# Performance work log

Measured on AMD Instinct MI355X. Metric: run time of the kernel, lower is better.

The kernel has to match this reference:

```python
import jax, jax.numpy as jnp
import numpy as np

V, E, H, T, C, B, S = 50000, 256, 512, 50, 5, 128, 512
FC1 = 500


def setup_inputs() -> dict:
    key = jax.random.key(0)
    ks = jax.random.split(key, 13)
    n = lambda i, shape, sc: (jax.random.normal(ks[i], shape, jnp.float32) * sc)
    return {
        "x": jax.random.randint(ks[0], (B, S), 0, V),
        "topic": n(1, (B, T), 1.0),
        "h0": n(2, (B, H), 1.0),
        "c0": n(3, (B, H), 1.0),
        "embed": n(4, (V, E), 0.05),
        "W_x": n(5, (E, 4 * H), 0.02),
        "W_t": n(6, (T, 4 * H), 0.02),
        "W_h": n(7, (H, 4 * H), 0.02),
        "b": jnp.zeros((4 * H,), jnp.float32),
        "fc1_w": n(8, (FC1, H), 0.02),
        "fc1_b": jnp.zeros((FC1,), jnp.float32),
        "fc2_w": n(9, (C, FC1), 0.02),
        "fc2_b": jnp.zeros((C,), jnp.float32),
    }


def reference(x, topic, h0, c0, embed, W_x, W_t, W_h, b, fc1_w, fc1_b, fc2_w, fc2_b):
    # Embedding lookup: [B,S,E] -> time-major [S,B,E]
    x_emb = jnp.transpose(embed[x], (1, 0, 2))
    # Precompute input + topic gate contributions (topic is constant per step)
    gx = jnp.einsum("sbe,eg->sbg", x_emb, W_x) + (topic @ W_t + b)[None]  # [S,B,4H]

    def step(carry, g):
        h, c = carry
        g = g + h @ W_h
        i, f, gg, o = jnp.split(g, 4, axis=-1)
        i = jax.nn.sigmoid(i)
        f = jax.nn.sigmoid(f)
        gg = jnp.tanh(gg)
        o = jax.nn.sigmoid(o)
        c = f * c + i * gg
        h = o * jnp.tanh(c)
        return (h, c), None

    (h_last, _), _ = jax.lax.scan(step, (h0, c0), gx)
    # MLP head (dropout = identity in eval)
    hid = h_last @ fc1_w.T + fc1_b
    logits = hid @ fc2_w.T + fc2_b
    return logits
```

## Files before the change

### kernel.cpp

```cpp
#include <hip/hip_runtime.h>
#include <hip/hip_bf16.h>

typedef unsigned short u16;
typedef unsigned int u32;
typedef __attribute__((ext_vector_type(8))) short short8;
typedef __attribute__((ext_vector_type(4))) float f32x4;


__device__ __forceinline__ float bf2f(u16 v){ union{u32 u; float f;} x; x.u = ((u32)v)<<16; return x.f; }
__device__ __forceinline__ u16 f2bf(float f){ union{float f; u32 u;} x; x.f = f; u32 r = ((x.u>>16)&1u) + 0x7FFFu; return (u16)((x.u + r)>>16); }
__device__ __forceinline__ float sigf(float x){ return 1.f/(1.f+__expf(-x)); }
__device__ __forceinline__ float tanh_f(float x){ return 2.f/(1.f+__expf(-2.f*x)) - 1.f; }

#define POLL_GUARD (1u<<14)


__global__ void k_prep(const float* __restrict__ Wh, const float* __restrict__ Wx,
                       u16* __restrict__ WhT, u16* __restrict__ WxT){
  __shared__ u16 tile[32][33];
  int b = blockIdx.x;
  const float* src; u16* dst; int K, kt, nt;
  if (b < 1024){ src = Wh; dst = WhT; K = 512; kt = b & 15; nt = b >> 4; }
  else { b -= 1024; src = Wx; dst = WxT; K = 256; kt = b & 7; nt = b >> 3; }
  int tx = threadIdx.x, ty = threadIdx.y;
  #pragma unroll
  for (int p = 0; p < 4; ++p){
    int r = p*8 + ty;
    tile[r][tx] = f2bf(src[(kt*32 + r)*2048 + nt*32 + tx]);
  }
  __syncthreads();
  #pragma unroll
  for (int p = 0; p < 4; ++p){
    int r = p*8 + ty;
    dst[(nt*32 + r)*K + kt*32 + tx] = tile[tx][r];
  }
}

__global__ void k_topic(const float* __restrict__ topic, const float* __restrict__ Wt,
                        const float* __restrict__ bias, float* __restrict__ tb){
  int b = blockIdx.y;
  int col = blockIdx.x*256 + threadIdx.x;
  float acc = bias[col];
  #pragma unroll 5
  for (int t = 0; t < 50; ++t)
    acc += topic[b*50 + t] * Wt[t*2048 + col];
  tb[b*2048 + col] = acc;
}

__global__ void k_init(const float* __restrict__ h0, u32* __restrict__ U){
  int uid = blockIdx.x*256 + threadIdx.x;
  int parity = (uid >= 12288) ? 1 : 0;
  int rem = uid - parity*12288;
  int g   = rem / 768;   int r2 = rem - g*768;
  int row = r2 / 96;     int p3 = r2 - row*96;
  int prod = p3 / 6;     int u  = p3 - prod*6;
  u32 d0=0, d1=0, d2=0, d3;
  if (parity == 0){
    const float* hr = h0 + (g*8 + row)*512 + prod*32 + u*6;
    int nv = 32 - u*6; if (nv > 6) nv = 6;
    u16 vals[6] = {0,0,0,0,0,0};
    for (int j = 0; j < nv; ++j) vals[j] = f2bf(hr[j]);
    d0 = (u32)vals[0] | ((u32)vals[1]<<16);
    d1 = (u32)vals[2] | ((u32)vals[3]<<16);
    d2 = (u32)vals[4] | ((u32)vals[5]<<16);
    d3 = 0u;
  } else {
    d3 = 0xFFFFFFFFu;
  }
  u32* dst = U + (size_t)uid*4;
  dst[0]=d0; dst[1]=d1; dst[2]=d2; dst[3]=d3;
}

__global__ void __launch_bounds__(256, 1)
k_rnn(const int* __restrict__ x, const float* __restrict__ embed, const float* __restrict__ c0,
      const u16* __restrict__ WhT, const u16* __restrict__ WxT, const float* __restrict__ tb,
      u32* __restrict__ U, float* __restrict__ hf)
{
  const int bx = blockIdx.x;
  const int g = bx & 15;
  const int w = bx >> 4;
  const int tid = threadIdx.x;
  const int v = tid >> 6;
  const int lane = tid & 63;
  const int l15 = lane & 15, l4 = lane >> 4;
  const int arr = l15 & 7;

  __shared__ __align__(16) u16 ldsH[8][704];
  __shared__ __align__(16) float ldsD[16][132];
  __shared__ int ldsX[8][512];
  __shared__ u16 ldsP[8][32];

  const int er = tid >> 5, ehc = tid & 31;
  const int eb = g*8 + er;
  const int ecol = w*32 + ehc;
  float c_val = c0[eb*512 + ecol];
  const float tb0 = tb[eb*2048 +    0 + ecol];
  const float tb1 = tb[eb*2048 +  512 + ecol];
  const float tb2 = tb[eb*2048 + 1024 + ecol];
  const float tb3 = tb[eb*2048 + 1536 + ecol];

  short8 b2[2][16], b1[2][8];
  #pragma unroll
  for (int j = 0; j < 2; ++j){
    const int cl = (2*v + j)*16 + l15;
    const int cg = (cl & 3)*512 + w*32 + (cl >> 2);
    #pragma unroll
    for (int kt = 0; kt < 16; ++kt)
      b2[j][kt] = *(const short8*)(WhT + cg*512 + kt*32 + l4*8);
    #pragma unroll
    for (int kt = 0; kt < 8; ++kt)
      b1[j][kt] = *(const short8*)(WxT + cg*256 + kt*32 + l4*8);
  }

  {
    const int4* src = (const int4*)(x + g*4096);
    int4* dst = (int4*)&ldsX[0][0];
    #pragma unroll
    for (int i = 0; i < 4; ++i) dst[tid + 256*i] = src[tid + 256*i];
  }
  __syncthreads();

  int rw0,rw1,rw2, cb0,cb1,cb2; u32 of0,of1,of2;
  {
    int pid, row, p3, prod, u;
    pid = tid*3 + 0; row = pid/96; p3 = pid - row*96; prod = p3/6; u = p3 - prod*6;
    rw0 = row; cb0 = prod*40 + u*6 + row*8; of0 = (u32)(((g*8+row)*16+prod)*6+u);
    pid = tid*3 + 1; row = pid/96; p3 = pid - row*96; prod = p3/6; u = p3 - prod*6;
    rw1 = row; cb1 = prod*40 + u*6 + row*8; of1 = (u32)(((g*8+row)*16+prod)*6+u);
    pid = tid*3 + 2; row = pid/96; p3 = pid - row*96; prod = p3/6; u = p3 - prod*6;
    rw2 = row; cb2 = prod*40 + u*6 + row*8; of2 = (u32)(((g*8+row)*16+prod)*6+u);
  }
  int pk_row=0, pk_ucol=0, pk_nv=0; u32 pk_off=0;
  if (tid < 48){
    pk_row = tid/6; int u = tid - pk_row*6;
    pk_ucol = u*6;
    pk_nv = 32 - pk_ucol; if (pk_nv > 6) pk_nv = 6;
    pk_off = (u32)(((g*8+pk_row)*16 + w)*6 + u);
  }
  int goff[16];
  #pragma unroll
  for (int kt = 0; kt < 16; ++kt) goff[kt] = kt*40 + l4*8 + arr*8;
  const u16* hrow = &ldsH[arr][0];

  short8 a1A[8], a1B[8];
  {
    const int idx0 = ldsX[arr][0];
    const float* ep = embed + (u32)idx0*256 + l4*8;
    #pragma unroll
    for (int kt = 0; kt < 8; ++kt){
      float4 f0 = *(const float4*)(ep + kt*32);
      float4 f1 = *(const float4*)(ep + kt*32 + 4);
      union { short8 s; u32 u[4]; } pk;
      asm("v_cvt_pk_bf16_f32 %0, %1, %2" : "=v"(pk.u[0]) : "v"(f0.x), "v"(f0.y));
      asm("v_cvt_pk_bf16_f32 %0, %1, %2" : "=v"(pk.u[1]) : "v"(f0.z), "v"(f0.w));
      asm("v_cvt_pk_bf16_f32 %0, %1, %2" : "=v"(pk.u[2]) : "v"(f1.x), "v"(f1.y));
      asm("v_cvt_pk_bf16_f32 %0, %1, %2" : "=v"(pk.u[3]) : "v"(f1.z), "v"(f1.w));
      a1A[kt] = pk.s;
    }
  }

  union F4 { f32x4 f; u32 u[4]; };

  auto step = [&](int t, short8 (&a1c)[8], short8 (&a1n)[8]){
    const int tn = (t < 511) ? t + 1 : 511;
    const int idxn = ldsX[arr][tn];
    const float* ep = embed + (u32)idxn*256 + l4*8;
    f32x4 e[16];
    #pragma unroll
    for (int kt = 0; kt < 8; ++kt){
      asm volatile("global_load_dwordx4 %0, %2, off\n\t"
                   "global_load_dwordx4 %1, %3, off"
                   : "=v"(e[2*kt]), "=v"(e[2*kt+1])
                   : "v"(ep + kt*32), "v"(ep + kt*32 + 4));
    }
    f32x4 aX0a = {0.f,0.f,0.f,0.f}, aX0b = {0.f,0.f,0.f,0.f};
    f32x4 aX1a = {0.f,0.f,0.f,0.f}, aX1b = {0.f,0.f,0.f,0.f};
    #pragma unroll
    for (int kt = 0; kt < 4; ++kt){
      aX0a = __builtin_amdgcn_mfma_f32_16x16x32_bf16(a1c[kt], b1[0][kt], aX0a, 0, 0, 0);
      aX1a = __builtin_amdgcn_mfma_f32_16x16x32_bf16(a1c[kt], b1[1][kt], aX1a, 0, 0, 0);
    }
    #pragma unroll
    for (int kt = 4; kt < 8; ++kt){
      aX0b = __builtin_amdgcn_mfma_f32_16x16x32_bf16(a1c[kt], b1[0][kt], aX0b, 0, 0, 0);
      aX1b = __builtin_amdgcn_mfma_f32_16x16x32_bf16(a1c[kt], b1[1][kt], aX1b, 0, 0, 0);
    }
    const f32x4 aX0 = aX0a + aX0b;
    const f32x4 aX1 = aX1a + aX1b;
    F4 H0,H1,H2;
    {
      const u32* b = U + (size_t)((t & 1)*12288)*4;
      const u32 *a0 = b + (size_t)of0*4, *a1_ = b + (size_t)of1*4, *a2 = b + (size_t)of2*4;
      const u32 tg = (u32)t;
      bool ok; u32 guard = 0;
      do {
        asm volatile(
          "global_load_dwordx4 %0, %3, off sc0 sc1\n\t"
          "global_load_dwordx4 %1, %4, off sc0 sc1\n\t"
          "global_load_dwordx4 %2, %5, off sc0 sc1\n\t"
          "s_waitcnt vmcnt(0)"
          : "=&v"(H0.f), "=&v"(H1.f), "=&v"(H2.f)
          : "v"(a0), "v"(a1_), "v"(a2)
          : "memory");
        int mine = (H0.u[3]==tg) && (H1.u[3]==tg) && (H2.u[3]==tg);
        ok = __all(mine) != 0;
      } while (!ok && ++guard < POLL_GUARD);
    }
    {
      u16* p;
      p = &ldsH[rw0][cb0]; *(u32*)p = H0.u[0]; *(u32*)(p+2) = H0.u[1]; *(u32*)(p+4) = H0.u[2];
      p = &ldsH[rw1][cb1]; *(u32*)p = H1.u[0]; *(u32*)(p+2) = H1.u[1]; *(u32*)(p+4) = H1.u[2];
      p = &ldsH[rw2][cb2]; *(u32*)p = H2.u[0]; *(u32*)(p+2) = H2.u[1]; *(u32*)(p+4) = H2.u[2];
    }
    __syncthreads();
    f32x4 c0a={0.f,0.f,0.f,0.f}, c0b={0.f,0.f,0.f,0.f}, c0c={0.f,0.f,0.f,0.f}, c0d={0.f,0.f,0.f,0.f};
    f32x4 c1a={0.f,0.f,0.f,0.f}, c1b={0.f,0.f,0.f,0.f}, c1c={0.f,0.f,0.f,0.f}, c1d={0.f,0.f,0.f,0.f};
    #pragma unroll
    for (int kt = 0; kt < 4; ++kt){
      short8 ah = *(const short8*)(hrow + goff[kt]);
      c0a = __builtin_amdgcn_mfma_f32_16x16x32_bf16(ah, b2[0][kt], c0a, 0, 0, 0);
      c1a = __builtin_amdgcn_mfma_f32_16x16x32_bf16(ah, b2[1][kt], c1a, 0, 0, 0);
    }
    #pragma unroll
    for (int kt = 4; kt < 8; ++kt){
      short8 ah = *(const short8*)(hrow + goff[kt]);
      c0b = __builtin_amdgcn_mfma_f32_16x16x32_bf16(ah, b2[0][kt], c0b, 0, 0, 0);
      c1b = __builtin_amdgcn_mfma_f32_16x16x32_bf16(ah, b2[1][kt], c1b, 0, 0, 0);
    }
    #pragma unroll
    for (int kt = 8; kt < 12; ++kt){
      short8 ah = *(const short8*)(hrow + goff[kt]);
      c0c = __builtin_amdgcn_mfma_f32_16x16x32_bf16(ah, b2[0][kt], c0c, 0, 0, 0);
      c1c = __builtin_amdgcn_mfma_f32_16x16x32_bf16(ah, b2[1][kt], c1c, 0, 0, 0);
    }
    #pragma unroll
    for (int kt = 12; kt < 16; ++kt){
      short8 ah = *(const short8*)(hrow + goff[kt]);
      c0d = __builtin_amdgcn_mfma_f32_16x16x32_bf16(ah, b2[0][kt], c0d, 0, 0, 0);
      c1d = __builtin_amdgcn_mfma_f32_16x16x32_bf16(ah, b2[1][kt], c1d, 0, 0, 0);
    }
    const f32x4 acc0 = (aX0 + (c0a + c0b)) + (c0c + c0d);
    const f32x4 acc1 = (aX1 + (c1a + c1b)) + (c1c + c1d);
    #pragma unroll
    for (int jj = 0; jj < 4; ++jj){
      ldsD[l4*4 + jj][(2*v + 0)*16 + l15] = acc0[jj];
      ldsD[l4*4 + jj][(2*v + 1)*16 + l15] = acc1[jj];
    }
    __syncthreads();
    const f32x4 pa = *(const f32x4*)&ldsD[er][ehc*4];
    const float iv = sigf(pa[0] + tb0);
    const float fv = sigf(pa[1] + tb1);
    const float gv = tanh_f(pa[2] + tb2);
    const float ov = sigf(pa[3] + tb3);
    c_val = fv*c_val + iv*gv;
    const float hval = ov*tanh_f(c_val);
    ldsP[er][ehc] = f2bf(hval);
    if (t == 511) hf[eb*512 + ecol] = hval;
    __syncthreads();
    if (t < 511 && tid < 48){
      u16 v0 = ldsP[pk_row][(pk_ucol+0) & 31];
      u16 v1 = ldsP[pk_row][(pk_ucol+1) & 31];
      u16 v2 = ldsP[pk_row][(pk_ucol+2) & 31];
      u16 v3 = ldsP[pk_row][(pk_ucol+3) & 31];
      u16 v4 = ldsP[pk_row][(pk_ucol+4) & 31];
      u16 v5 = ldsP[pk_row][(pk_ucol+5) & 31];
      if (pk_nv < 6){ v2 = 0; v3 = 0; v4 = 0; v5 = 0; }
      F4 D;
      D.u[0] = (u32)v0 | ((u32)v1<<16);
      D.u[1] = (u32)v2 | ((u32)v3<<16);
      D.u[2] = (u32)v4 | ((u32)v5<<16);
      D.u[3] = (u32)(t + 1);
      u32* dst = U + (size_t)(((u32)((t+1)&1))*12288 + pk_off)*4;
      asm volatile("global_store_dwordx4 %0, %1, off sc0 sc1" :: "v"(dst), "v"(D.f) : "memory");
    }
    #pragma unroll
    for (int kt = 0; kt < 8; ++kt){
      union { short8 s; u32 u[4]; } pk;
      asm volatile("v_cvt_pk_bf16_f32 %0, %1, %2" : "=v"(pk.u[0]) : "v"(e[2*kt][0]),   "v"(e[2*kt][1]));
      asm volatile("v_cvt_pk_bf16_f32 %0, %1, %2" : "=v"(pk.u[1]) : "v"(e[2*kt][2]),   "v"(e[2*kt][3]));
      asm volatile("v_cvt_pk_bf16_f32 %0, %1, %2" : "=v"(pk.u[2]) : "v"(e[2*kt+1][0]), "v"(e[2*kt+1][1]));
      asm volatile("v_cvt_pk_bf16_f32 %0, %1, %2" : "=v"(pk.u[3]) : "v"(e[2*kt+1][2]), "v"(e[2*kt+1][3]));
      a1n[kt] = pk.s;
    }
  };

  for (int t = 0; t < 512; t += 2){
    step(t,     a1A, a1B);
    step(t + 1, a1B, a1A);
  }
}

__global__ void k_head1(const float* __restrict__ hf, const float* __restrict__ w1,
                        const float* __restrict__ b1v, float* __restrict__ hid){
  int b = blockIdx.y;
  int j = blockIdx.x*256 + threadIdx.x;
  if (j >= 500) return;
  float acc = b1v[j];
  const float* hr = hf + b*512;
  const float* wr = w1 + j*512;
  for (int k = 0; k < 512; ++k) acc += hr[k]*wr[k];
  hid[b*500 + j] = acc;
}

__global__ void k_head2(const float* __restrict__ hid, const float* __restrict__ w2,
                        const float* __restrict__ b2v, float* __restrict__ out){
  int o = blockIdx.x*256 + threadIdx.x;
  if (o >= 640) return;
  int b = o / 5, cls = o % 5;
  float acc = b2v[cls];
  const float* hr = hid + b*500;
  const float* wr = w2 + cls*500;
  for (int j = 0; j < 500; ++j) acc += hr[j]*wr[j];
  out[o] = acc;
}

extern "C" void kernel_launch(void* const* d_in, const int* in_sizes, int n_in,
                              void* d_out, int out_size, void* d_ws, size_t ws_size,
                              hipStream_t stream) {
  const int*   x     = (const int*)d_in[0];
  const float* topic = (const float*)d_in[1];
  const float* h0    = (const float*)d_in[2];
  const float* c0    = (const float*)d_in[3];
  const float* embed = (const float*)d_in[4];
  const float* Wx    = (const float*)d_in[5];
  const float* Wt    = (const float*)d_in[6];
  const float* Wh    = (const float*)d_in[7];
  const float* bias  = (const float*)d_in[8];
  const float* fc1w  = (const float*)d_in[9];
  const float* fc1b  = (const float*)d_in[10];
  const float* fc2w  = (const float*)d_in[11];
  const float* fc2b  = (const float*)d_in[12];

  char* ws = (char*)d_ws;
  u16*   WhT = (u16*)(ws + 0);
  u16*   WxT = (u16*)(ws + 2097152);
  float* tb  = (float*)(ws + 3145728);
  u32*   U   = (u32*)(ws + 4194304);
  float* hf  = (float*)(ws + 4980736);
  float* hid = (float*)(ws + 3145728);

  k_prep<<<dim3(1536), dim3(32, 8), 0, stream>>>(Wh, Wx, WhT, WxT);
  k_topic<<<dim3(8, 128), dim3(256), 0, stream>>>(topic, Wt, bias, tb);
  k_init<<<dim3(96), dim3(256), 0, stream>>>(h0, U);

  k_rnn<<<dim3(256), dim3(256), 0, stream>>>(x, embed, c0, WhT, WxT, tb, U, hf);

  k_head1<<<dim3(2, 128), dim3(256), 0, stream>>>(hf, fc1w, fc1b, hid);
  k_head2<<<dim3(3), dim3(256), 0, stream>>>(hid, fc2w, fc2b, (float*)d_out);
}
```

Baseline: 1.757 ms.

## Halve RNN workgroups by giving each block 64 hidden columns with 512 threads

The persistent LSTM kernel now runs 128 blocks of 512 threads instead of 256 blocks of 256. Each block owns 64 hidden columns rather than 32, and the h-exchange loads, pack/publish logic and LDS scratch are resized to match. This halves the number of blocks that must poll and synchronise through global memory each timestep. In exchange each block carries more work per step and more threads wait at every barrier. An explicit vmcnt wait is also added after the publish store.

```diff
diff --git a/kernel.cpp b/kernel.cpp
--- a/kernel.cpp
+++ b/kernel.cpp
@@ -71,7 +71,7 @@
   dst[0]=d0; dst[1]=d1; dst[2]=d2; dst[3]=d3;
 }
 
-__global__ void __launch_bounds__(256, 1)
+__global__ void __launch_bounds__(512, 1)
 k_rnn(const int* __restrict__ x, const float* __restrict__ embed, const float* __restrict__ c0,
       const u16* __restrict__ WhT, const u16* __restrict__ WxT, const float* __restrict__ tb,
       u32* __restrict__ U, float* __restrict__ hf)
@@ -86,13 +86,13 @@
   const int arr = l15 & 7;
 
   __shared__ __align__(16) u16 ldsH[8][704];
-  __shared__ __align__(16) float ldsD[16][132];
+  __shared__ __align__(16) float ldsD[16][260];
   __shared__ int ldsX[8][512];
-  __shared__ u16 ldsP[8][32];
-
-  const int er = tid >> 5, ehc = tid & 31;
+  __shared__ u16 ldsP[8][64];
+
+  const int er = tid >> 6, ehc = tid & 63;
   const int eb = g*8 + er;
-  const int ecol = w*32 + ehc;
+  const int ecol = w*64 + ehc;
   float c_val = c0[eb*512 + ecol];
   const float tb0 = tb[eb*2048 +    0 + ecol];
   const float tb1 = tb[eb*2048 +  512 + ecol];
@@ -103,7 +103,7 @@
   #pragma unroll
   for (int j = 0; j < 2; ++j){
     const int cl = (2*v + j)*16 + l15;
-    const int cg = (cl & 3)*512 + w*32 + (cl >> 2);
+    const int cg = (cl & 3)*512 + w*64 + (cl >> 2);
     #pragma unroll
     for (int kt = 0; kt < 16; ++kt)
       b2[j][kt] = *(const short8*)(WhT + cg*512 + kt*32 + l4*8);
@@ -116,26 +116,25 @@
     const int4* src = (const int4*)(x + g*4096);
     int4* dst = (int4*)&ldsX[0][0];
     #pragma unroll
-    for (int i = 0; i < 4; ++i) dst[tid + 256*i] = src[tid + 256*i];
+    for (int i = 0; i < 2; ++i) dst[tid + 512*i] = src[tid + 512*i];
   }
   __syncthreads();
 
-  int rw0,rw1,rw2, cb0,cb1,cb2; u32 of0,of1,of2;
+  int rw0,rw1, cb0,cb1; u32 of0,of1;
   {
     int pid, row, p3, prod, u;
-    pid = tid*3 + 0; row = pid/96; p3 = pid - row*96; prod = p3/6; u = p3 - prod*6;
+    pid = tid;       row = pid/96; p3 = pid - row*96; prod = p3/6; u = p3 - prod*6;
     rw0 = row; cb0 = prod*40 + u*6 + row*8; of0 = (u32)(((g*8+row)*16+prod)*6+u);
-    pid = tid*3 + 1; row = pid/96; p3 = pid - row*96; prod = p3/6; u = p3 - prod*6;
+    pid = tid + 384; row = pid/96; p3 = pid - row*96; prod = p3/6; u = p3 - prod*6;
     rw1 = row; cb1 = prod*40 + u*6 + row*8; of1 = (u32)(((g*8+row)*16+prod)*6+u);
-    pid = tid*3 + 2; row = pid/96; p3 = pid - row*96; prod = p3/6; u = p3 - prod*6;
-    rw2 = row; cb2 = prod*40 + u*6 + row*8; of2 = (u32)(((g*8+row)*16+prod)*6+u);
-  }
-  int pk_row=0, pk_ucol=0, pk_nv=0; u32 pk_off=0;
-  if (tid < 48){
-    pk_row = tid/6; int u = tid - pk_row*6;
+  }
+  int pk_row=0, pk_ucol=0, pk_nv=0, pk_lp=0; u32 pk_off=0;
+  if (tid < 96){
+    pk_row = tid/12; int rem = tid - pk_row*12;
+    pk_lp = rem/6; int u = rem - pk_lp*6;
     pk_ucol = u*6;
     pk_nv = 32 - pk_ucol; if (pk_nv > 6) pk_nv = 6;
-    pk_off = (u32)(((g*8+pk_row)*16 + w)*6 + u);
+    pk_off = (u32)(((g*8+pk_row)*16 + (w*2+pk_lp))*6 + u);
   }
   int goff[16];
   #pragma unroll
@@ -187,30 +186,26 @@
     }
     const f32x4 aX0 = aX0a + aX0b;
     const f32x4 aX1 = aX1a + aX1b;
-    F4 H0,H1,H2;
-    {
+    if (tid < 384){
+      F4 H0,H1;
       const u32* b = U + (size_t)((t & 1)*12288)*4;
-      const u32 *a0 = b + (size_t)of0*4, *a1_ = b + (size_t)of1*4, *a2 = b + (size_t)of2*4;
+      const u32 *a0 = b + (size_t)of0*4, *a1_ = b + (size_t)of1*4;
       const u32 tg = (u32)t;
       bool ok; u32 guard = 0;
       do {
         asm volatile(
-          "global_load_dwordx4 %0, %3, off sc0 sc1\n\t"
-          "global_load_dwordx4 %1, %4, off sc0 sc1\n\t"
-          "global_load_dwordx4 %2, %5, off sc0 sc1\n\t"
+          "global_load_dwordx4 %0, %2, off sc0 sc1\n\t"
+          "global_load_dwordx4 %1, %3, off sc0 sc1\n\t"
           "s_waitcnt vmcnt(0)"
-          : "=&v"(H0.f), "=&v"(H1.f), "=&v"(H2.f)
-          : "v"(a0), "v"(a1_), "v"(a2)
+          : "=&v"(H0.f), "=&v"(H1.f)
+          : "v"(a0), "v"(a1_)
           : "memory");
-        int mine = (H0.u[3]==tg) && (H1.u[3]==tg) && (H2.u[3]==tg);
+        int mine = (H0.u[3]==tg) && (H1.u[3]==tg);
         ok = __all(mine) != 0;
       } while (!ok && ++guard < POLL_GUARD);
-    }
-    {
       u16* p;
       p = &ldsH[rw0][cb0]; *(u32*)p = H0.u[0]; *(u32*)(p+2) = H0.u[1]; *(u32*)(p+4) = H0.u[2];
       p = &ldsH[rw1][cb1]; *(u32*)p = H1.u[0]; *(u32*)(p+2) = H1.u[1]; *(u32*)(p+4) = H1.u[2];
-      p = &ldsH[rw2][cb2]; *(u32*)p = H2.u[0]; *(u32*)(p+2) = H2.u[1]; *(u32*)(p+4) = H2.u[2];
     }
     __syncthreads();
     f32x4 c0a={0.f,0.f,0.f,0.f}, c0b={0.f,0.f,0.f,0.f}, c0c={0.f,0.f,0.f,0.f}, c0d={0.f,0.f,0.f,0.f};
@@ -257,13 +252,14 @@
     ldsP[er][ehc] = f2bf(hval);
     if (t == 511) hf[eb*512 + ecol] = hval;
     __syncthreads();
-    if (t < 511 && tid < 48){
-      u16 v0 = ldsP[pk_row][(pk_ucol+0) & 31];
-      u16 v1 = ldsP[pk_row][(pk_ucol+1) & 31];
-      u16 v2 = ldsP[pk_row][(pk_ucol+2) & 31];
-      u16 v3 = ldsP[pk_row][(pk_ucol+3) & 31];
-      u16 v4 = ldsP[pk_row][(pk_ucol+4) & 31];
-      u16 v5 = ldsP[pk_row][(pk_ucol+5) & 31];
+    if (t < 511 && tid < 96){
+      const int cbase = pk_lp*32;
+      u16 v0 = ldsP[pk_row][cbase + ((pk_ucol+0) & 31)];
+      u16 v1 = ldsP[pk_row][cbase + ((pk_ucol+1) & 31)];
+      u16 v2 = ldsP[pk_row][cbase + ((pk_ucol+2) & 31)];
+      u16 v3 = ldsP[pk_row][cbase + ((pk_ucol+3) & 31)];
+      u16 v4 = ldsP[pk_row][cbase + ((pk_ucol+4) & 31)];
+      u16 v5 = ldsP[pk_row][cbase + ((pk_ucol+5) & 31)];
       if (pk_nv < 6){ v2 = 0; v3 = 0; v4 = 0; v5 = 0; }
       F4 D;
       D.u[0] = (u32)v0 | ((u32)v1<<16);
@@ -273,6 +269,7 @@
       u32* dst = U + (size_t)(((u32)((t+1)&1))*12288 + pk_off)*4;
       asm volatile("global_store_dwordx4 %0, %1, off sc0 sc1" :: "v"(dst), "v"(D.f) : "memory");
     }
+    asm volatile("s_waitcnt vmcnt(0)" ::: "memory");
     #pragma unroll
     for (int kt = 0; kt < 8; ++kt){
       union { short8 s; u32 u[4]; } pk;
@@ -343,7 +340,7 @@
   k_topic<<<dim3(8, 128), dim3(256), 0, stream>>>(topic, Wt, bias, tb);
   k_init<<<dim3(96), dim3(256), 0, stream>>>(h0, U);
 
-  k_rnn<<<dim3(256), dim3(256), 0, stream>>>(x, embed, c0, WhT, WxT, tb, U, hf);
+  k_rnn<<<dim3(128), dim3(512), 0, stream>>>(x, embed, c0, WhT, WxT, tb, U, hf);
 
   k_head1<<<dim3(2, 128), dim3(256), 0, stream>>>(hf, fc1w, fc1b, hid);
   k_head2<<<dim3(3), dim3(256), 0, stream>>>(hid, fc2w, fc2b, (float*)d_out);
```

Measured after the change: 5.348 ms. +204.3%, slower.
